# Kernel tuning notes

Hardware: AMD Instinct MI355X
Metric: run time of the kernel (lower is better)

The kernel has to match this reference:

```python
import jax, jax.numpy as jnp
import numpy as np

B, T = 128, 2048
N_IN, N_H, N_OUT = 16, 128, 5
I_DECAY, V_DECAY = 1024, 128          # Loihi 12-bit decay constants
ALPHA_I = (4096 - I_DECAY) / 4096.0   # current decay multiplier
ALPHA_V = (4096 - V_DECAY) / 4096.0   # voltage decay multiplier
W_SCALE = 64.0                        # Loihi synaptic weight scaling (1 << 6)
THETA = 1 * 64.0                      # vThMant * (1 << 6)
SCALE_RHO, TAU_RHO = 1.0, 1.0
SG_TAU = TAU_RHO * THETA              # surrogate-gradient width


@jax.custom_vjp
def spike_fn(x):
    # Heaviside spike with SLAYER exponential surrogate gradient
    return (x >= 0).astype(x.dtype)

def _spike_fwd(x):
    return spike_fn(x), x

def _spike_bwd(x, g):
    return (g * (SCALE_RHO / SG_TAU) * jnp.exp(-jnp.abs(x) / SG_TAU),)

spike_fn.defvjp(_spike_fwd, _spike_bwd)


def weight_norm(v, g):
    # torch weight_norm with dim=0: per-output-row normalization
    return g[:, None] * v / jnp.linalg.norm(v, axis=1, keepdims=True)


def loihi_spikes(z):
    # z: (B, O, T) synaptic input. Sequential Loihi CUBA integrate-and-fire.
    zt = jnp.transpose(z, (2, 0, 1))  # (T, B, O)

    def step(carry, zin):
        u, v = carry
        u = ALPHA_I * u + zin          # synaptic current
        v = ALPHA_V * v + u            # membrane voltage
        s = spike_fn(v - THETA)
        v = v * (1.0 - s)              # reset-to-zero on spike
        return (u, v), s

    init = (jnp.zeros(zt.shape[1:], zt.dtype), jnp.zeros(zt.shape[1:], zt.dtype))
    _, s = jax.lax.scan(step, init, zt)
    return jnp.transpose(s, (1, 2, 0))  # (B, O, T)


def delay_shift1(x):
    # shift spikes one timestep later (slayer.delayShift(spike, 1))
    return jnp.concatenate([jnp.zeros_like(x[..., :1]), x[..., :-1]], axis=-1)


def axon_delay(x, d):
    # per-channel fractional delay via linear interpolation; x: (B,C,T), d: (C,)
    Tn = x.shape[-1]
    d0 = jnp.floor(d)
    f = (d - d0)[None, :, None]
    d0i = d0.astype(jnp.int32)
    t = jnp.arange(Tn, dtype=jnp.int32)

    def gather(shift):
        idx = t[None, :] - shift[:, None]          # (C, T)
        g = jnp.take_along_axis(
            x, jnp.broadcast_to(jnp.clip(idx, 0, Tn - 1)[None], x.shape), axis=-1)
        return jnp.where((idx >= 0)[None], g, 0.0)

    return (1.0 - f) * gather(d0i) + f * gather(d0i + 1)


def setup_inputs() -> dict:
    key = jax.random.key(0)
    ks = jax.random.split(key, 8)
    spike = (jax.random.uniform(ks[0], (B, N_IN, T)) < 0.1).astype(jnp.float32)
    fc1_v = jax.random.normal(ks[1], (N_H, N_IN), jnp.float32)
    fc2_v = jax.random.normal(ks[2], (N_H, N_H), jnp.float32)
    fc3_v = jax.random.normal(ks[3], (N_OUT, N_H), jnp.float32)
    # weight_norm init: g = ||v|| so W == v initially
    fc1_g = jnp.linalg.norm(fc1_v, axis=1)
    fc2_g = jnp.linalg.norm(fc2_v, axis=1)
    fc3_g = jnp.linalg.norm(fc3_v, axis=1)
    delay1 = jax.random.uniform(ks[4], (N_H,), jnp.float32) * 10.0
    delay2 = jax.random.uniform(ks[5], (N_H,), jnp.float32) * 10.0
    return {"spike": spike, "fc1_v": fc1_v, "fc1_g": fc1_g, "fc2_v": fc2_v,
            "fc2_g": fc2_g, "fc3_v": fc3_v, "fc3_g": fc3_g,
            "delay1": delay1, "delay2": delay2}


def reference(spike, fc1_v, fc1_g, fc2_v, fc2_g, fc3_v, fc3_g, delay1, delay2):
    x = spike.reshape(spike.shape[0], -1, spike.shape[-1])  # (B, 16, T)
    counts = []

    s = loihi_spikes(W_SCALE * jnp.einsum('oc,bct->bot', weight_norm(fc1_v, fc1_g), x))
    s = delay_shift1(s)
    counts.append(jnp.sum(s))
    s = axon_delay(s, delay1)

    s = loihi_spikes(W_SCALE * jnp.einsum('oc,bct->bot', weight_norm(fc2_v, fc2_g), s))
    s = delay_shift1(s)
    counts.append(jnp.sum(s))
    s = axon_delay(s, delay2)

    s = loihi_spikes(W_SCALE * jnp.einsum('oc,bct->bot', weight_norm(fc3_v, fc3_g), s))
    s = delay_shift1(s)
    counts.append(jnp.sum(s))

    return s, jnp.stack(counts).reshape(1, 3)
```

## Files before the change

kernel.cpp:

```cpp
#include <hip/hip_runtime.h>
#include <cstdint>

#define B_    128
#define T_    2048
#define NIN_  16
#define NH_   128
#define NOUT_ 5

#define ALPHA_I_ 0.75f
#define ALPHA_V_ 0.96875f
#define THETA_   64.0f

#define NCHUNK_ 8
#define CHT_    256
#define WARM_   96

typedef short bf16x8 __attribute__((ext_vector_type(8)));
typedef float f32x16 __attribute__((ext_vector_type(16)));
typedef int   i32x2  __attribute__((ext_vector_type(2)));

__device__ __forceinline__ float mulrn(float a, float b) { return __fmul_rn(a, b); }
__device__ __forceinline__ float addrn(float a, float b) { return __fadd_rn(a, b); }

__device__ __forceinline__ uint16_t f2bf(float x) {
  uint32_t u = __float_as_uint(x);
  return (uint16_t)((u + 0x7FFFu + ((u >> 16) & 1u)) >> 16);
}

__device__ __forceinline__ bf16x8 expand8v(uint32_t byt) {
  union { uint32_t w[4]; bf16x8 f; } r;
#pragma unroll
  for (int j = 0; j < 4; j++) {
    uint32_t b0 = (byt >> (2 * j)) & 1u;
    uint32_t b1 = (byt >> (2 * j + 1)) & 1u;
    r.w[j] = (b0 ? 0x3F80u : 0u) | (b1 ? 0x3F800000u : 0u);
  }
  return r.f;
}

__global__ __launch_bounds__(1024) void prep_pack_kernel(
    const float* __restrict__ spike, uint16_t* __restrict__ Xb,
    const float* __restrict__ fc1_v, const float* __restrict__ fc1_g,
    const float* __restrict__ fc2_v, const float* __restrict__ fc2_g,
    const float* __restrict__ fc3_v, const float* __restrict__ fc3_g,
    const float* __restrict__ delay1, const float* __restrict__ delay2,
    uint16_t* __restrict__ w1swz, uint16_t* __restrict__ wswz,
    float* __restrict__ w3T, float4* __restrict__ efo1, float4* __restrict__ efo2,
    float* __restrict__ counts) {
  int tid = threadIdx.x;
  if (blockIdx.x < 256) {
    int gw = blockIdx.x * 16 + (tid >> 6);
    int lane = tid & 63;
    int b = gw >> 5;
    int t = (gw & 31) * 64 + lane;
    const float* sp = spike + (size_t)b * NIN_ * T_ + t;
    uint32_t mask = 0;
#pragma unroll
    for (int c = 0; c < NIN_; c++) {
      unsigned long long bal = __ballot(sp[(size_t)c * T_] != 0.f);
      mask |= (uint32_t)((bal >> lane) & 1ull) << c;
    }
    Xb[(size_t)b * T_ + t] = (uint16_t)mask;
    return;
  }
  __shared__ float s_n1[NH_], s_n2[NH_], s_n3[8], s_g2[NH_];
  {
    int o = tid >> 3, sub = tid & 7;
    float ss = 0.f;
    for (int c = sub; c < NIN_; c += 8) { float v = fc1_v[o * NIN_ + c]; ss = __fmaf_rn(v, v, ss); }
    ss += __shfl_down(ss, 4, 64); ss += __shfl_down(ss, 2, 64); ss += __shfl_down(ss, 1, 64);
    if (sub == 0) s_n1[o] = sqrtf(ss);
    float ss2 = 0.f;
    for (int c = sub; c < NH_; c += 8) { float v = fc2_v[o * NH_ + c]; ss2 = __fmaf_rn(v, v, ss2); }
    ss2 += __shfl_down(ss2, 4, 64); ss2 += __shfl_down(ss2, 2, 64); ss2 += __shfl_down(ss2, 1, 64);
    if (sub == 0) s_n2[o] = sqrtf(ss2);
  }
  if (tid < NOUT_ * 8) {
    int o = tid >> 3, sub = tid & 7;
    float ss = 0.f;
    for (int c = sub; c < NH_; c += 8) { float v = fc3_v[o * NH_ + c]; ss = __fmaf_rn(v, v, ss); }
    ss += __shfl_down(ss, 4, 64); ss += __shfl_down(ss, 2, 64); ss += __shfl_down(ss, 1, 64);
    if (sub == 0) s_n3[o] = sqrtf(ss);
  }
  if (tid < NH_) s_g2[tid] = fc2_g[tid];
  if (tid < 3) counts[tid] = 0.f;
  __syncthreads();

  if (tid < NH_) {
    float d1 = delay1[tid];
    float fl = floorf(d1);
    float f = __fsub_rn(d1, fl);
    efo1[tid] = make_float4(__int_as_float((int)fl + 1), f, __fsub_rn(1.0f, f), 0.f);
    float d2 = delay2[tid];
    float fl2 = floorf(d2);
    float f2v = __fsub_rn(d2, fl2);
    efo2[tid] = make_float4(__int_as_float((int)fl2 + 1), f2v, __fsub_rn(1.0f, f2v), 0.f);
    w3T[tid * 8 + 5] = f2v;
    w3T[tid * 8 + 6] = __fsub_rn(1.0f, f2v);
    w3T[tid * 8 + 7] = 0.f;
  }
  for (int i = tid; i < NH_ * NIN_; i += 1024) {
    int o = i >> 4, c = i & 15;
    float wv = 64.0f * __fdiv_rn(mulrn(fc1_g[o], fc1_v[i]), s_n1[o]);
    int mt = o >> 5, lane = (o & 31) + 32 * ((c >> 3) & 1), j = c & 7;
    w1swz[(mt * 64 + lane) * 8 + j] = f2bf(wv);
  }
  for (int i = tid; i < NH_ * NH_; i += 1024) {
    int o = i >> 7, c = i & 127;
    float wv = 64.0f * __fdiv_rn(mulrn(s_g2[o], fc2_v[i]), s_n2[o]);
    float d1 = delay1[c];
    float f = __fsub_rn(d1, floorf(d1));
    int lane = (o & 31) + 32 * ((c >> 3) & 1);
    int ks = c >> 4, j = c & 7, mt = o >> 5;
    wswz[((size_t)((0 * 4 + mt) * 8 + ks) * 64 + lane) * 8 + j] = f2bf(__fmul_rn(wv, f));
    wswz[((size_t)((1 * 4 + mt) * 8 + ks) * 64 + lane) * 8 + j] =
        f2bf(__fmul_rn(wv, __fsub_rn(1.0f, f)));
  }
  for (int i = tid; i < NOUT_ * NH_; i += 1024) {
    int o = i / NH_, c = i & 127;
    float wv = 64.0f * __fdiv_rn(mulrn(fc3_g[o], fc3_v[i]), s_n3[o]);
    w3T[c * 8 + o] = wv;
  }
}

#define GATHER_AND_SCAN(aA, aB, hi, u, v, m)                               \
  {                                                                        \
    m = 0u;                                                                \
    _Pragma("unroll") for (int k = 0; k < 4; k++) {                        \
      float ev[4], od[4];                                                  \
      _Pragma("unroll") for (int i = 0; i < 4; i++) {                      \
        i32x2 pr_ = __builtin_amdgcn_permlane32_swap(                      \
            __float_as_int(aA[4 * k + i]), __float_as_int(aB[4 * k + i]),  \
            false, false);                                                 \
        ev[i] = __int_as_float(pr_[0]);                                    \
        od[i] = __int_as_float(pr_[1]);                                    \
      }                                                                    \
      _Pragma("unroll") for (int tt = 0; tt < 8; tt++) {                   \
        float z = (tt < 4) ? ev[tt & 3] : od[tt & 3];                      \
        u = addrn(mulrn(ALPHA_I_, u), z);                                  \
        v = addrn(mulrn(ALPHA_V_, v), u);                                  \
        bool sbit = (v >= THETA_);                                         \
        v = sbit ? 0.f : v;                                                \
        m |= sbit ? (1u << (8 * k + tt)) : 0u;                             \
      }                                                                    \
    }                                                                      \
  }

#define EMIT_PT(m, m_prev, e_o, ptw, chwstart)                             \
  {                                                                        \
    uint32_t sm = (uint32_t)((((uint64_t)(m) << 32) | (m_prev)) >> (32 - (e_o))); \
    uint32_t myword = 0u;                                                  \
    _Pragma("unroll") for (int j = 0; j < 32; j++) {                       \
      unsigned long long bal_ = __ballot((int)(sm << (31 - j)) < 0);       \
      uint32_t w_ = hi ? (uint32_t)(bal_ >> 32) : (uint32_t)bal_;          \
      myword = (tl == j) ? w_ : myword;                                    \
    }                                                                      \
    ptw[(size_t)(1 + (chwstart) + tl) * 4 + (pair * 2 + hi)] = myword;     \
  }

__global__ __launch_bounds__(128, 2) void fused_layer1(const uint16_t* __restrict__ Xb,
                                                       const uint16_t* __restrict__ w1swz,
                                                       const float4* __restrict__ efo,
                                                       uint32_t* __restrict__ PT1,
                                                       float* __restrict__ cnt) {
  int tid = threadIdx.x;
  int pair = tid >> 6, lane = tid & 63;
  int hi = lane >> 5, tl = lane & 31;
  int ci = blockIdx.x, b = blockIdx.y;
  const bf16x8* w1v = (const bf16x8*)w1swz;
  bf16x8 wA = w1v[(pair * 2 + 0) * 64 + lane];
  bf16x8 wB = w1v[(pair * 2 + 1) * 64 + lane];
  int e_o = __float_as_int(efo[tid].x);

  int wch = (ci == 0) ? 0 : (WARM_ / 32);
  int nch = CHT_ / 32 + wch;
  int chbase0 = ci * CHT_ - wch * 32;
  const uint16_t* xb = Xb + (size_t)b * T_;
  uint32_t* ptw = PT1 + (size_t)b * (T_ + 1) * 4;

  f32x16 zacc;
#pragma unroll
  for (int r = 0; r < 16; r++) zacc[r] = 0.f;

  float u = 0.f, v = 0.f, csum = 0.f;
  uint32_t m_prev = 0u;
  uint32_t x = xb[chbase0 + tl];
  for (int g = 0; g < nch; g++) {
    uint32_t xn = (g + 1 < nch) ? (uint32_t)xb[chbase0 + (g + 1) * 32 + tl] : 0u;
    uint32_t byt = (x >> (8 * hi)) & 0xFFu;
    bf16x8 e = expand8v(byt);
    f32x16 aA, aB;
    aA = __builtin_amdgcn_mfma_f32_32x32x16_bf16(e, wA, zacc, 0, 0, 0);
    aB = __builtin_amdgcn_mfma_f32_32x32x16_bf16(e, wB, zacc, 0, 0, 0);
    uint32_t m;
    GATHER_AND_SCAN(aA, aB, hi, u, v, m);
    if (g >= wch) {
      int chwstart = chbase0 + g * 32;
      EMIT_PT(m, m_prev, e_o, ptw, chwstart);
      int gw = chwstart >> 5;
      int pc = __popc(m);
      if (gw == 63) pc -= (int)(m >> 31);
      csum += (float)pc;
    }
    m_prev = m;
    x = xn;
  }
  if (ci == 0 && tid < 4) ptw[tid] = 0u;
  for (int off = 32; off; off >>= 1) csum += __shfl_down(csum, off, 64);
  if (lane == 0) atomicAdd(cnt, csum);
}

__global__ __launch_bounds__(128, 2) void fused_layer2(const uint32_t* __restrict__ PT1,
                                                       const uint16_t* __restrict__ wswz,
                                                       const float4* __restrict__ efo,
                                                       uint32_t* __restrict__ PT2,
                                                       float* __restrict__ cnt) {
  int tid = threadIdx.x;
  int pair = tid >> 6, lane = tid & 63;
  int hi = lane >> 5, tl = lane & 31;
  int ci = blockIdx.x, b = blockIdx.y;
  const bf16x8* wsv = (const bf16x8*)wswz;
  int mtA = pair * 2, mtB = pair * 2 + 1;
  bf16x8 wfA[8], woA[8], wfB[8], woB[8];
#pragma unroll
  for (int ks = 0; ks < 8; ks++) {
    wfA[ks] = wsv[((size_t)((0 * 4 + mtA) * 8 + ks) * 64) + lane];
    woA[ks] = wsv[((size_t)((1 * 4 + mtA) * 8 + ks) * 64) + lane];
    wfB[ks] = wsv[((size_t)((0 * 4 + mtB) * 8 + ks) * 64) + lane];
    woB[ks] = wsv[((size_t)((1 * 4 + mtB) * 8 + ks) * 64) + lane];
  }
  int e_o = __float_as_int(efo[tid].x);

  int wch = (ci == 0) ? 0 : (WARM_ / 32);
  int nch = CHT_ / 32 + wch;
  int chbase0 = ci * CHT_ - wch * 32;
  const uint4* pt = (const uint4*)PT1 + (size_t)b * (T_ + 1);
  uint32_t* ptw = PT2 + (size_t)b * (T_ + 1) * 4;

  float u = 0.f, v = 0.f, csum = 0.f;
  uint32_t m_prev = 0u;
  uint4 R0 = pt[chbase0 + tl];
  uint4 R1 = pt[chbase0 + tl + 1];
  for (int g = 0; g < nch; g++) {
    uint4 R0n = R0, R1n = R1;
    if (g + 1 < nch) {
      R0n = pt[chbase0 + (g + 1) * 32 + tl];
      R1n = pt[chbase0 + (g + 1) * 32 + tl + 1];
    }
    uint32_t r0w[4] = {R0.x, R0.y, R0.z, R0.w};
    uint32_t r1w[4] = {R1.x, R1.y, R1.z, R1.w};
    f32x16 aA, aB;
#pragma unroll
    for (int r = 0; r < 16; r++) { aA[r] = 0.f; aB[r] = 0.f; }
#pragma unroll
    for (int ks = 0; ks < 8; ks++) {
      int sh = 16 * (ks & 1) + 8 * hi;
      uint32_t b0 = (r0w[ks >> 1] >> sh) & 0xFFu;
      uint32_t b1 = (r1w[ks >> 1] >> sh) & 0xFFu;
      bf16x8 e0 = expand8v(b0);
      bf16x8 e1 = expand8v(b1);
      aA = __builtin_amdgcn_mfma_f32_32x32x16_bf16(e0, wfA[ks], aA, 0, 0, 0);
      aA = __builtin_amdgcn_mfma_f32_32x32x16_bf16(e1, woA[ks], aA, 0, 0, 0);
      aB = __builtin_amdgcn_mfma_f32_32x32x16_bf16(e0, wfB[ks], aB, 0, 0, 0);
      aB = __builtin_amdgcn_mfma_f32_32x32x16_bf16(e1, woB[ks], aB, 0, 0, 0);
    }
    uint32_t m;
    GATHER_AND_SCAN(aA, aB, hi, u, v, m);
    if (g >= wch) {
      int chwstart = chbase0 + g * 32;
      EMIT_PT(m, m_prev, e_o, ptw, chwstart);
      int gw = chwstart >> 5;
      int pc = __popc(m);
      if (gw == 63) pc -= (int)(m >> 31);
      csum += (float)pc;
    }
    m_prev = m;
    R0 = R0n; R1 = R1n;
  }
  if (ci == 0 && tid < 4) ptw[tid] = 0u;
  for (int off = 32; off; off >>= 1) csum += __shfl_down(csum, off, 64);
  if (lane == 0) atomicAdd(cnt, csum);
}

__global__ __launch_bounds__(256) void gemm3_kernel(const uint32_t* __restrict__ PTpad,
                                                    const float* __restrict__ w3T,
                                                    float* __restrict__ z) {
  int tid = threadIdx.x;
  int t = blockIdx.x * 256 + tid;
  int b = blockIdx.y;
  const uint4* pt = (const uint4*)PTpad + (size_t)b * (T_ + 1);
  uint4 R0 = pt[t];
  uint4 R1 = pt[t + 1];
  uint32_t r0w[4] = {R0.x, R0.y, R0.z, R0.w};
  uint32_t r1w[4] = {R1.x, R1.y, R1.z, R1.w};

  float acc[NOUT_];
#pragma unroll
  for (int o = 0; o < NOUT_; o++) acc[o] = 0.f;

#pragma unroll
  for (int c = 0; c < NH_; c++) {
    const float* wc = w3T + (c << 3);
    float f = wc[5], omf = wc[6];
    float fb0 = (float)((r0w[c >> 5] >> (c & 31)) & 1u);
    float fb1 = (float)((r1w[c >> 5] >> (c & 31)) & 1u);
    float val = __fmaf_rn(omf, fb1, __fmul_rn(f, fb0));
#pragma unroll
    for (int o = 0; o < NOUT_; o++) acc[o] = __fmaf_rn(wc[o], val, acc[o]);
  }

#pragma unroll
  for (int o = 0; o < NOUT_; o++)
    z[((size_t)b * NOUT_ + o) * T_ + t] = acc[o];
}

__global__ __launch_bounds__(64) void scan3_kernel(const float* __restrict__ z3,
                                                   float* __restrict__ out,
                                                   float* __restrict__ cnt) {
  int id = blockIdx.x * 64 + threadIdx.x;
  int row = id % (B_ * NOUT_);
  int ci = id / (B_ * NOUT_);
  int tstart = ci * CHT_;
  int t0 = (ci == 0) ? 0 : tstart - WARM_;
  const float4* zp4 = (const float4*)(z3 + (size_t)row * T_);

  float u = 0.f, v = 0.f, carry = 0.f;
  int cnt_i = 0;
  for (int gg = t0 / 16; gg < tstart / 16; gg++) {
#pragma unroll
    for (int q = 0; q < 4; q++) {
      float4 cv = zp4[gg * 4 + q];
      float zv[4] = {cv.x, cv.y, cv.z, cv.w};
#pragma unroll
      for (int j = 0; j < 4; j++) {
        u = addrn(mulrn(ALPHA_I_, u), zv[j]);
        v = addrn(mulrn(ALPHA_V_, v), u);
        bool s = (v >= THETA_);
        v = s ? 0.f : v;
        carry = s ? 1.f : 0.f;
      }
    }
  }
  float4* op4 = (float4*)(out + (size_t)row * T_ + tstart);
  for (int gg = 0; gg < CHT_ / 16; gg++) {
    float sarr[16];
#pragma unroll
    for (int q = 0; q < 4; q++) {
      float4 cv = zp4[(tstart / 16 + gg) * 4 + q];
      float zv[4] = {cv.x, cv.y, cv.z, cv.w};
#pragma unroll
      for (int j = 0; j < 4; j++) {
        u = addrn(mulrn(ALPHA_I_, u), zv[j]);
        v = addrn(mulrn(ALPHA_V_, v), u);
        bool s = (v >= THETA_);
        v = s ? 0.f : v;
        sarr[q * 4 + j] = s ? 1.f : 0.f;
      }
    }
#pragma unroll
    for (int k = 0; k < 16; k++) {
      int t = tstart + gg * 16 + k;
      if (t < T_ - 1) cnt_i += (sarr[k] != 0.f) ? 1 : 0;
    }
    op4[gg * 4 + 0] = make_float4(carry, sarr[0], sarr[1], sarr[2]);
    op4[gg * 4 + 1] = make_float4(sarr[3], sarr[4], sarr[5], sarr[6]);
    op4[gg * 4 + 2] = make_float4(sarr[7], sarr[8], sarr[9], sarr[10]);
    op4[gg * 4 + 3] = make_float4(sarr[11], sarr[12], sarr[13], sarr[14]);
    carry = sarr[15];
  }
  float c = (float)cnt_i;
  for (int off = 32; off; off >>= 1) c += __shfl_down(c, off, 64);
  if ((threadIdx.x & 63) == 0) atomicAdd(cnt, c);
}

extern "C" void kernel_launch(void* const* d_in, const int* in_sizes, int n_in,
                              void* d_out, int out_size, void* d_ws, size_t ws_size,
                              hipStream_t stream) {
  (void)in_sizes; (void)n_in; (void)out_size; (void)ws_size;
  const float* spike  = (const float*)d_in[0];
  const float* fc1_v  = (const float*)d_in[1];
  const float* fc1_g  = (const float*)d_in[2];
  const float* fc2_v  = (const float*)d_in[3];
  const float* fc2_g  = (const float*)d_in[4];
  const float* fc3_v  = (const float*)d_in[5];
  const float* fc3_g  = (const float*)d_in[6];
  const float* delay1 = (const float*)d_in[7];
  const float* delay2 = (const float*)d_in[8];
  float* out = (float*)d_out;

  float* ws = (float*)d_ws;
  float* w3T       = ws;
  float4* efo1     = (float4*)(ws + 1024);
  float4* efo2     = (float4*)(ws + 1536);
  uint16_t* w1swz  = (uint16_t*)(ws + 2048);
  uint16_t* wswz   = (uint16_t*)(ws + 3072);
  uint16_t* Xb     = (uint16_t*)(ws + 19456);
  uint32_t* PT1    = (uint32_t*)(ws + 150528);
  uint32_t* PT2    = (uint32_t*)(ws + 1264640);
  float* z3        = ws + 2313728;
  float* counts = out + (size_t)B_ * NOUT_ * T_;

  prep_pack_kernel<<<dim3(257), 1024, 0, stream>>>(
      spike, Xb, fc1_v, fc1_g, fc2_v, fc2_g, fc3_v, fc3_g,
      delay1, delay2, w1swz, wswz, w3T, efo1, efo2, counts);

  fused_layer1<<<dim3(NCHUNK_, B_), 128, 0, stream>>>(Xb, w1swz, efo1, PT1, counts + 0);

  fused_layer2<<<dim3(NCHUNK_, B_), 128, 0, stream>>>(PT1, wswz, efo2, PT2, counts + 1);

  gemm3_kernel<<<dim3(T_ / 256, B_), 256, 0, stream>>>(PT2, w3T, z3);
  scan3_kernel<<<dim3(NCHUNK_ * B_ * NOUT_ / 64), 64, 0, stream>>>(z3, out, counts + 2);
}
```

Measured before the change: 205.2 us.

## Replace per-channel FMA loop in gemm3 with nibble lookup tables in LDS

The layer-3 GEMM kernel now builds a per-block shared-memory table holding the precomputed 5-output weighted sums for every 4-bit pattern of spikes, for both interpolation taps. The inner loop then does 32 table lookups per tap instead of 128 per-channel FMAs. This cuts ALU work but adds LDS table construction in every block plus a barrier. It also changes the floating-point summation order, which may shift results near the spike threshold.

```diff
diff --git a/kernel.cpp b/kernel.cpp
--- a/kernel.cpp
+++ b/kernel.cpp
@@ -285,7 +285,29 @@
 __global__ __launch_bounds__(256) void gemm3_kernel(const uint32_t* __restrict__ PTpad,
                                                     const float* __restrict__ w3T,
                                                     float* __restrict__ z) {
+  __shared__ float s_lut[2 * 32 * 16 * 8];
   int tid = threadIdx.x;
+  for (int e = tid; e < 2 * 32 * 16; e += 256) {
+    int tap = e >> 9, rem = e & 511, np = rem >> 4, nib = rem & 15;
+    float a0 = 0.f, a1 = 0.f, a2 = 0.f, a3 = 0.f, a4 = 0.f;
+#pragma unroll
+    for (int j = 0; j < 4; j++) {
+      if ((nib >> j) & 1) {
+        int c = np * 4 + j;
+        float fs = w3T[c * 8 + (tap ? 6 : 5)];
+        a0 = __fmaf_rn(__fmul_rn(w3T[c * 8 + 0], fs), 1.0f, a0);
+        a1 = __fmaf_rn(__fmul_rn(w3T[c * 8 + 1], fs), 1.0f, a1);
+        a2 = __fmaf_rn(__fmul_rn(w3T[c * 8 + 2], fs), 1.0f, a2);
+        a3 = __fmaf_rn(__fmul_rn(w3T[c * 8 + 3], fs), 1.0f, a3);
+        a4 = __fmaf_rn(__fmul_rn(w3T[c * 8 + 4], fs), 1.0f, a4);
+      }
+    }
+    float* dst = s_lut + e * 8;
+    dst[0] = a0; dst[1] = a1; dst[2] = a2; dst[3] = a3; dst[4] = a4;
+    dst[5] = 0.f; dst[6] = 0.f; dst[7] = 0.f;
+  }
+  __syncthreads();
+
   int t = blockIdx.x * 256 + tid;
   int b = blockIdx.y;
   const uint4* pt = (const uint4*)PTpad + (size_t)b * (T_ + 1);
@@ -294,24 +316,30 @@
   uint32_t r0w[4] = {R0.x, R0.y, R0.z, R0.w};
   uint32_t r1w[4] = {R1.x, R1.y, R1.z, R1.w};
 
-  float acc[NOUT_];
-#pragma unroll
-  for (int o = 0; o < NOUT_; o++) acc[o] = 0.f;
-
-#pragma unroll
-  for (int c = 0; c < NH_; c++) {
-    const float* wc = w3T + (c << 3);
-    float f = wc[5], omf = wc[6];
-    float fb0 = (float)((r0w[c >> 5] >> (c & 31)) & 1u);
-    float fb1 = (float)((r1w[c >> 5] >> (c & 31)) & 1u);
-    float val = __fmaf_rn(omf, fb1, __fmul_rn(f, fb0));
-#pragma unroll
-    for (int o = 0; o < NOUT_; o++) acc[o] = __fmaf_rn(wc[o], val, acc[o]);
-  }
-
-#pragma unroll
-  for (int o = 0; o < NOUT_; o++)
-    z[((size_t)b * NOUT_ + o) * T_ + t] = acc[o];
+  float acc0 = 0.f, acc1 = 0.f, acc2 = 0.f, acc3 = 0.f, acc4 = 0.f;
+#pragma unroll
+  for (int np = 0; np < 32; np++) {
+    uint32_t nib0 = (r0w[np >> 3] >> ((np & 7) * 4)) & 15u;
+    uint32_t nib1 = (r1w[np >> 3] >> ((np & 7) * 4)) & 15u;
+    const float* e0 = s_lut + ((np * 16 + (int)nib0) << 3);
+    const float* e1 = s_lut + ((512 * 8) >> 3 << 3) + (((512 + np * 16 + (int)nib1) - 512) << 3) + 512 * 8 - 512 * 8;
+    e1 = s_lut + ((512 + np * 16 + (int)nib1) << 3);
+    float4 v0 = *(const float4*)(e0);
+    float w40 = e0[4];
+    float4 v1 = *(const float4*)(e1);
+    float w41 = e1[4];
+    acc0 = addrn(acc0, addrn(v0.x, v1.x));
+    acc1 = addrn(acc1, addrn(v0.y, v1.y));
+    acc2 = addrn(acc2, addrn(v0.z, v1.z));
+    acc3 = addrn(acc3, addrn(v0.w, v1.w));
+    acc4 = addrn(acc4, addrn(w40, w41));
+  }
+
+  z[((size_t)b * NOUT_ + 0) * T_ + t] = acc0;
+  z[((size_t)b * NOUT_ + 1) * T_ + t] = acc1;
+  z[((size_t)b * NOUT_ + 2) * T_ + t] = acc2;
+  z[((size_t)b * NOUT_ + 3) * T_ + t] = acc3;
+  z[((size_t)b * NOUT_ + 4) * T_ + t] = acc4;
 }
 
 __global__ __launch_bounds__(64) void scan3_kernel(const float* __restrict__ z3,
```

Result: faster. 193.0 us (-6.0%).
